# Kernel tuning notes

Hardware: AMD Instinct MI355X
Metric: run time of the kernel (lower is better)

## Reference

```python
import jax, jax.numpy as jnp
import numpy as np

VOCAB, T, IN, H, L = 32000, 4096, 512, 256, 2


def setup_inputs() -> dict:
    key = jax.random.key(0)
    ks = jax.random.split(key, 32)
    inp = {}
    inp["tokens"] = jax.random.randint(ks[0], (T,), 0, VOCAB)
    inp["emb"] = jax.random.normal(ks[1], (VOCAB, IN), dtype=jnp.float32) * 0.02
    i = 2
    for d in ("f", "b"):
        for l in range(L):
            in_l = IN if l == 0 else H
            inp[f"{d}_Wih{l}"] = jax.random.normal(ks[i], (4 * H, in_l), dtype=jnp.float32) * 0.05; i += 1
            inp[f"{d}_Whh{l}"] = jax.random.normal(ks[i], (4 * H, H), dtype=jnp.float32) * 0.05; i += 1
            inp[f"{d}_bih{l}"] = jnp.zeros((4 * H,), dtype=jnp.float32)
            inp[f"{d}_bhh{l}"] = jnp.zeros((4 * H,), dtype=jnp.float32)
    return inp


def _lstm_layer(x_seq, Wih, Whh, bih, bhh):
    # x_seq: [T, in]; torch.nn.LSTMCell gate order: i, f, g, o
    Hh = Whh.shape[1]
    b = bih + bhh
    def step(carry, x):
        h, c = carry
        g = x @ Wih.T + h @ Whh.T + b           # [4H]
        i_, f_, g_, o_ = jnp.split(g, 4)
        c = jax.nn.sigmoid(f_) * c + jax.nn.sigmoid(i_) * jnp.tanh(g_)
        h = jax.nn.sigmoid(o_) * jnp.tanh(c)
        return (h, c), h
    z = jnp.zeros((Hh,), x_seq.dtype)
    (h, c), hs = jax.lax.scan(step, (z, z), x_seq)
    return hs, h, c                              # [T,H], [H], [H]


def _run_dir(x_seq, params):
    finals = []
    h_seq = x_seq
    for (Wih, Whh, bih, bhh) in params:
        h_seq, h, c = _lstm_layer(h_seq, Wih, Whh, bih, bhh)
        finals.append((c, h))
    return h_seq, finals


def reference(tokens, emb,
              f_Wih0, f_Whh0, f_bih0, f_bhh0, f_Wih1, f_Whh1, f_bih1, f_bhh1,
              b_Wih0, b_Whh0, b_bih0, b_bhh0, b_Wih1, b_Whh1, b_bih1, b_bhh1):
    x = emb[tokens]                              # [T, IN] embedding lookup
    fparams = [(f_Wih0, f_Whh0, f_bih0, f_bhh0), (f_Wih1, f_Whh1, f_bih1, f_bhh1)]
    bparams = [(b_Wih0, b_Whh0, b_bih0, b_bhh0), (b_Wih1, b_Whh1, b_bih1, b_bhh1)]
    f_out, f_fin = _run_dir(x, fparams)          # forward over sequence
    b_out_rev, b_fin = _run_dir(x[::-1], bparams)  # backward over reversed sequence
    b_out = b_out_rev[::-1]
    outputs = jnp.concatenate([f_out, b_out], axis=-1)  # [T, 2H]
    cell_memories = jnp.stack([jnp.stack([f_fin[l][0], b_fin[l][0]]) for l in range(L)])  # [L,2,H]
    hidden_states = jnp.stack([jnp.stack([f_fin[l][1], b_fin[l][1]]) for l in range(L)])  # [L,2,H]
    return cell_memories, hidden_states, outputs
```

## Files before the change

kernel.cpp:

```cpp
#include <hip/hip_runtime.h>
#include <math.h>

#define T_SEQ 4096
#define NWG_LAUNCH 512

__device__ __forceinline__ float sigmoidf_(float x) {
  return 1.0f / (1.0f + expf(-x));
}

__device__ __forceinline__ unsigned long long pack_h(int tag, float h) {
  return ((unsigned long long)(unsigned)tag << 32) |
         (unsigned long long)__float_as_uint(h);
}

__device__ __forceinline__ unsigned long long ld_sc0(const unsigned long long* p) {
  unsigned long long v;
  asm volatile("global_load_dwordx2 %0, %1, off sc0\n\ts_waitcnt vmcnt(0)"
               : "=v"(v) : "v"(p) : "memory");
  return v;
}
__device__ __forceinline__ unsigned long long ld_mall(const unsigned long long* p) {
  unsigned long long v;
  asm volatile("global_load_dwordx2 %0, %1, off sc0 sc1\n\ts_waitcnt vmcnt(0)"
               : "=v"(v) : "v"(p) : "memory");
  return v;
}
__device__ __forceinline__ void st_pub(unsigned long long* p, unsigned long long v) {
  asm volatile("global_store_dwordx2 %0, %1, off sc0\n\t"
               "global_store_dwordx2 %0, %1, off sc0 sc1"
               :: "v"(p), "v"(v) : "memory");
}
__device__ __forceinline__ float poll_h(const unsigned long long* p, unsigned want) {
  int it = 0;
  for (;;) {
    unsigned long long v = ((it & 3) == 3) ? ld_mall(p) : ld_sc0(p);
    if ((unsigned)(v >> 32) == want) return __uint_as_float((unsigned)v);
    ++it;
  }
}

__global__ void gather_emb(const int* __restrict__ tokens,
                           const float4* __restrict__ emb4,
                           float4* __restrict__ X4) {
  int i = blockIdx.x * 256 + threadIdx.x;
  int t = i >> 7;
  int q = i & 127;
  X4[i] = emb4[(long)tokens[t] * 128 + q];
}

__global__ __launch_bounds__(256) void gemm_proj(
    const float* __restrict__ Xf, const float* __restrict__ Xb, int revb,
    const float* __restrict__ Wf, const float* __restrict__ Wb,
    const float* __restrict__ bihf, const float* __restrict__ bhhf,
    const float* __restrict__ bihb, const float* __restrict__ bhhb,
    float* __restrict__ Pf, float* __restrict__ Pb, int K)
{
  const int dirb = blockIdx.z;
  const float* X  = dirb ? Xb : Xf;
  const float* W  = dirb ? Wb : Wf;
  const float* bih = dirb ? bihb : bihf;
  const float* bhh = dirb ? bhhb : bhhf;
  float* Pp = dirb ? Pb : Pf;
  const int rev = dirb ? revb : 0;

  const int bn = blockIdx.x;
  const int bm = blockIdx.y;
  const int tid = threadIdx.x;
  const int tx = tid & 15, ty = tid >> 4;

  __shared__ float Xs[16][68];
  __shared__ float Ws[16][68];

  float acc[4][4] = {{0.f}};

  const int lrow = tid >> 2;
  const int lk4  = (tid & 3) * 4;
  const int xrow = bm * 64 + lrow;
  const int xsrc = rev ? (4095 - xrow) : xrow;
  const float* xptr = X + (long)xsrc * K + lk4;
  const float* wptr = W + (long)(bn * 64 + lrow) * K + lk4;

  for (int k0 = 0; k0 < K; k0 += 16) {
    float4 xv = *(const float4*)(xptr + k0);
    float4 wv = *(const float4*)(wptr + k0);
    __syncthreads();
    Xs[lk4 + 0][lrow] = xv.x; Xs[lk4 + 1][lrow] = xv.y;
    Xs[lk4 + 2][lrow] = xv.z; Xs[lk4 + 3][lrow] = xv.w;
    Ws[lk4 + 0][lrow] = wv.x; Ws[lk4 + 1][lrow] = wv.y;
    Ws[lk4 + 2][lrow] = wv.z; Ws[lk4 + 3][lrow] = wv.w;
    __syncthreads();
    #pragma unroll
    for (int kk = 0; kk < 16; ++kk) {
      float4 a = *(const float4*)(&Xs[kk][ty * 4]);
      float4 b = *(const float4*)(&Ws[kk][tx * 4]);
      acc[0][0] = fmaf(a.x, b.x, acc[0][0]); acc[0][1] = fmaf(a.x, b.y, acc[0][1]);
      acc[0][2] = fmaf(a.x, b.z, acc[0][2]); acc[0][3] = fmaf(a.x, b.w, acc[0][3]);
      acc[1][0] = fmaf(a.y, b.x, acc[1][0]); acc[1][1] = fmaf(a.y, b.y, acc[1][1]);
      acc[1][2] = fmaf(a.y, b.z, acc[1][2]); acc[1][3] = fmaf(a.y, b.w, acc[1][3]);
      acc[2][0] = fmaf(a.z, b.x, acc[2][0]); acc[2][1] = fmaf(a.z, b.y, acc[2][1]);
      acc[2][2] = fmaf(a.z, b.z, acc[2][2]); acc[2][3] = fmaf(a.z, b.w, acc[2][3]);
      acc[3][0] = fmaf(a.w, b.x, acc[3][0]); acc[3][1] = fmaf(a.w, b.y, acc[3][1]);
      acc[3][2] = fmaf(a.w, b.z, acc[3][2]); acc[3][3] = fmaf(a.w, b.w, acc[3][3]);
    }
  }

  const int c0 = bn * 64 + tx * 4;
  #pragma unroll
  for (int i = 0; i < 4; ++i) {
    const int r = bm * 64 + ty * 4 + i;
    float4 o4;
    o4.x = acc[i][0] + bih[c0 + 0] + bhh[c0 + 0];
    o4.y = acc[i][1] + bih[c0 + 1] + bhh[c0 + 1];
    o4.z = acc[i][2] + bih[c0 + 2] + bhh[c0 + 2];
    o4.w = acc[i][3] + bih[c0 + 3] + bhh[c0 + 3];
    *(float4*)(&Pp[(long)r * 1024 + c0]) = o4;
  }
}

__global__ __launch_bounds__(512, 2) void lstm_fused(
    const float* __restrict__ P0f, const float* __restrict__ P0b,
    const float* __restrict__ Whh0f, const float* __restrict__ Whh0b,
    const float* __restrict__ Wih1f, const float* __restrict__ Whh1f,
    const float* __restrict__ bih1f, const float* __restrict__ bhh1f,
    const float* __restrict__ Wih1b, const float* __restrict__ Whh1b,
    const float* __restrict__ bih1b, const float* __restrict__ bhh1b,
    float* __restrict__ out,
    unsigned long long* __restrict__ ring0,
    unsigned long long* __restrict__ h1x,
    int* __restrict__ flags)
{
  const int t = threadIdx.x;

  __shared__ int role_s;
  if (t == 0) {
    int xcd;
    asm volatile("s_getreg_b32 %0, hwreg(20, 0, 32)" : "=s"(xcd));
    xcd &= 7;
    int role = -1;
    const int lo = (xcd == 0) ? 0 : (xcd == 1 ? 12 : -1);
    if (lo >= 0) {
      for (int r = lo; r < lo + 12 && role < 0; ++r)
        if (atomicCAS(&flags[r], 0, 1) == 0) role = r;
    }
    const int n = atomicAdd(&flags[24], 1) + 1;
    if (role < 0 && n > NWG_LAUNCH - 32) {
      for (int r = 0; r < 24 && role < 0; ++r)
        if (atomicCAS(&flags[r], 0, 1) == 0) role = r;
    }
    role_s = role;
  }
  __syncthreads();
  const int role = role_s;
  if (role < 0) return;

  const int d   = role < 12 ? 0 : 1;
  const int sub = role < 12 ? role : role - 12;

  __shared__ float hx[512];
  __shared__ float lds_c[64];
  __shared__ float part[8 * 264];

  if (t < 64) lds_c[t] = 0.0f;

  unsigned long long* ring = ring0 + (long)d * T_SEQ * 256;

  if (sub < 4) {
    const int w = sub;
    const float* __restrict__ P = d ? P0b : P0f;
    const float* __restrict__ W = d ? Whh0b : Whh0f;

    const int kb = t >> 6;
    const int jg = t & 63;

    float wreg[128];
    #pragma unroll
    for (int jj = 0; jj < 4; ++jj) {
      const int m = jg * 4 + jj;
      const int j = (m >> 6) * 256 + w * 64 + (m & 63);
      const float4* wrow = (const float4*)(W + (long)j * 256 + kb * 32);
      #pragma unroll
      for (int kq = 0; kq < 8; ++kq) {
        float4 v = wrow[kq];
        wreg[jj * 32 + kq * 4 + 0] = v.x;
        wreg[jj * 32 + kq * 4 + 1] = v.y;
        wreg[jj * 32 + kq * 4 + 2] = v.z;
        wreg[jj * 32 + kq * 4 + 3] = v.w;
      }
    }

    const int cell = w * 64 + (t & 63);
    const long pbase = (long)(t & 63) + w * 64;

    for (int s = 0; s < T_SEQ; ++s) {
      float p0 = 0.f, p1 = 0.f, p2 = 0.f, p3 = 0.f;
      if (t < 64) {
        const float* prow = P + (long)s * 1024 + pbase;
        p0 = prow[0]; p1 = prow[256]; p2 = prow[512]; p3 = prow[768];
      }

      if (s == 0) {
        if (t < 256) hx[t] = 0.0f;
      } else if (t < 256) {
        hx[t] = poll_h(ring + (long)(s - 1) * 256 + t, (unsigned)s);
      }
      __syncthreads();

      float a0 = 0.f, a1 = 0.f, a2 = 0.f, a3 = 0.f;
      const float4* h4 = (const float4*)&hx[kb * 32];
      #pragma unroll
      for (int kq = 0; kq < 8; ++kq) {
        float4 hv = h4[kq];
        a0 = fmaf(wreg[0 * 32 + kq * 4 + 0], hv.x, a0);
        a0 = fmaf(wreg[0 * 32 + kq * 4 + 1], hv.y, a0);
        a0 = fmaf(wreg[0 * 32 + kq * 4 + 2], hv.z, a0);
        a0 = fmaf(wreg[0 * 32 + kq * 4 + 3], hv.w, a0);
        a1 = fmaf(wreg[1 * 32 + kq * 4 + 0], hv.x, a1);
        a1 = fmaf(wreg[1 * 32 + kq * 4 + 1], hv.y, a1);
        a1 = fmaf(wreg[1 * 32 + kq * 4 + 2], hv.z, a1);
        a1 = fmaf(wreg[1 * 32 + kq * 4 + 3], hv.w, a1);
        a2 = fmaf(wreg[2 * 32 + kq * 4 + 0], hv.x, a2);
        a2 = fmaf(wreg[2 * 32 + kq * 4 + 1], hv.y, a2);
        a2 = fmaf(wreg[2 * 32 + kq * 4 + 2], hv.z, a2);
        a2 = fmaf(wreg[2 * 32 + kq * 4 + 3], hv.w, a2);
        a3 = fmaf(wreg[3 * 32 + kq * 4 + 0], hv.x, a3);
        a3 = fmaf(wreg[3 * 32 + kq * 4 + 1], hv.y, a3);
        a3 = fmaf(wreg[3 * 32 + kq * 4 + 2], hv.z, a3);
        a3 = fmaf(wreg[3 * 32 + kq * 4 + 3], hv.w, a3);
      }
      float4 av; av.x = a0; av.y = a1; av.z = a2; av.w = a3;
      *(float4*)(&part[kb * 264 + jg * 4]) = av;
      __syncthreads();

      if (t < 64) {
        float s0 = p0, s1 = p1, s2 = p2, s3 = p3;
        #pragma unroll
        for (int q = 0; q < 8; ++q) {
          s0 += part[q * 264 + t];
          s1 += part[q * 264 + 64 + t];
          s2 += part[q * 264 + 128 + t];
          s3 += part[q * 264 + 192 + t];
        }
        float c = sigmoidf_(s1) * lds_c[t] + sigmoidf_(s0) * tanhf(s2);
        float h = sigmoidf_(s3) * tanhf(c);
        lds_c[t] = c;
        st_pub(ring + (long)s * 256 + cell, pack_h(s + 1, h));
        if (s == T_SEQ - 1) {
          out[d * 256 + cell] = c;
          out[1024 + d * 256 + cell] = h;
        }
      }
    }
  } else {
    const int w1 = sub - 4;
    const float* __restrict__ Wih = d ? Wih1b : Wih1f;
    const float* __restrict__ Whh = d ? Whh1b : Whh1f;
    const float* __restrict__ bih = d ? bih1b : bih1f;
    const float* __restrict__ bhh = d ? bhh1b : bhh1f;
    unsigned long long* slot = h1x + d * 512;
    float* hout = d ? (out + 2048 + (long)4095 * 512 + 256) : (out + 2048);
    const long hstr = d ? -512 : 512;

    const int kb = t >> 6;
    const int jg = t & 63;

    float wreg[2][64];
    #pragma unroll
    for (int rr = 0; rr < 2; ++rr) {
      const int m = jg * 2 + rr;
      const int j = (m >> 5) * 256 + w1 * 32 + (m & 31);
      const float* srcw = (kb < 4) ? (Wih + (long)j * 256 + kb * 64)
                                   : (Whh + (long)j * 256 + (kb - 4) * 64);
      const float4* s4 = (const float4*)srcw;
      #pragma unroll
      for (int q = 0; q < 16; ++q) {
        float4 v = s4[q];
        wreg[rr][q * 4 + 0] = v.x; wreg[rr][q * 4 + 1] = v.y;
        wreg[rr][q * 4 + 2] = v.z; wreg[rr][q * 4 + 3] = v.w;
      }
    }

    const int cell = w1 * 32 + (t & 31);
    float b0 = 0.f, b1 = 0.f, b2 = 0.f, b3 = 0.f;
    if (t < 32) {
      b0 = bih[cell] + bhh[cell];
      b1 = bih[256 + cell] + bhh[256 + cell];
      b2 = bih[512 + cell] + bhh[512 + cell];
      b3 = bih[768 + cell] + bhh[768 + cell];
    }

    for (int s = 0; s < T_SEQ; ++s) {
      if (t < 256) {
        hx[t] = poll_h(ring + (long)s * 256 + t, (unsigned)(s + 1));
      } else {
        hx[t] = poll_h(slot + ((s + 1) & 1) * 256 + (t - 256), (unsigned)s);
      }
      __syncthreads();

      float a0 = 0.f, a1 = 0.f;
      const float4* h4 = (const float4*)&hx[kb * 64];
      #pragma unroll
      for (int q = 0; q < 16; ++q) {
        float4 hv = h4[q];
        a0 = fmaf(wreg[0][q * 4 + 0], hv.x, a0);
        a0 = fmaf(wreg[0][q * 4 + 1], hv.y, a0);
        a0 = fmaf(wreg[0][q * 4 + 2], hv.z, a0);
        a0 = fmaf(wreg[0][q * 4 + 3], hv.w, a0);
        a1 = fmaf(wreg[1][q * 4 + 0], hv.x, a1);
        a1 = fmaf(wreg[1][q * 4 + 1], hv.y, a1);
        a1 = fmaf(wreg[1][q * 4 + 2], hv.z, a1);
        a1 = fmaf(wreg[1][q * 4 + 3], hv.w, a1);
      }
      float2 av2; av2.x = a0; av2.y = a1;
      *(float2*)(&part[kb * 264 + jg * 2]) = av2;
      __syncthreads();

      if (t < 32) {
        float s0 = b0, s1 = b1, s2 = b2, s3 = b3;
        #pragma unroll
        for (int q = 0; q < 8; ++q) {
          s0 += part[q * 264 + t];
          s1 += part[q * 264 + 32 + t];
          s2 += part[q * 264 + 64 + t];
          s3 += part[q * 264 + 96 + t];
        }
        float c = sigmoidf_(s1) * lds_c[t] + sigmoidf_(s0) * tanhf(s2);
        float h = sigmoidf_(s3) * tanhf(c);
        lds_c[t] = c;
        st_pub(&slot[(s & 1) * 256 + cell], pack_h(s + 1, h));
        hout[(long)s * hstr + cell] = h;
        if (s == T_SEQ - 1) {
          out[512 + d * 256 + cell] = c;
          out[1024 + 512 + d * 256 + cell] = h;
        }
      }
    }
  }
}

extern "C" void kernel_launch(void* const* d_in, const int* in_sizes, int n_in,
                              void* d_out, int out_size, void* d_ws, size_t ws_size,
                              hipStream_t stream) {
  const int*   tokens = (const int*)d_in[0];
  const float* emb    = (const float*)d_in[1];
  const float* fWih0 = (const float*)d_in[2];
  const float* fWhh0 = (const float*)d_in[3];
  const float* fbih0 = (const float*)d_in[4];
  const float* fbhh0 = (const float*)d_in[5];
  const float* fWih1 = (const float*)d_in[6];
  const float* fWhh1 = (const float*)d_in[7];
  const float* fbih1 = (const float*)d_in[8];
  const float* fbhh1 = (const float*)d_in[9];
  const float* bWih0 = (const float*)d_in[10];
  const float* bWhh0 = (const float*)d_in[11];
  const float* bbih0 = (const float*)d_in[12];
  const float* bbhh0 = (const float*)d_in[13];
  const float* bWih1 = (const float*)d_in[14];
  const float* bWhh1 = (const float*)d_in[15];
  const float* bbih1 = (const float*)d_in[16];
  const float* bbhh1 = (const float*)d_in[17];

  float* out = (float*)d_out;
  float* ws  = (float*)d_ws;

  float* X   = ws;
  float* P0f = ws + 4194304;
  float* P0b = ws + 8388608;
  unsigned long long* ring0 = (unsigned long long*)ws;
  unsigned long long* h1x   = (unsigned long long*)(ws + 12582912);
  int* flags = (int*)(ws + 12584960);

  gather_emb<<<2048, 256, 0, stream>>>(tokens, (const float4*)emb, (float4*)X);

  gemm_proj<<<dim3(16, 64, 2), 256, 0, stream>>>(
      X, X, 1, fWih0, bWih0, fbih0, fbhh0, bbih0, bbhh0, P0f, P0b, 512);

  hipMemsetAsync(ring0, 0, (size_t)2 * T_SEQ * 256 * sizeof(unsigned long long), stream);
  hipMemsetAsync(h1x, 0, 1024 * sizeof(unsigned long long) + 32 * sizeof(int), stream);

  lstm_fused<<<dim3(NWG_LAUNCH), 512, 0, stream>>>(
      P0f, P0b, fWhh0, bWhh0,
      fWih1, fWhh1, fbih1, fbhh1,
      bWih1, bWhh1, bbih1, bbhh1,
      out, ring0, h1x, flags);
}
```

Baseline: 7.026 ms.

## Double persistent LSTM workgroups per direction and parallelize gate activations

Splits each direction's recurrent work across 24 workgroups instead of 12: 8 for layer 0 with 32 cells each and 16 for layer 1 with 16 cells each. Each thread now holds fewer weight registers, and the gate nonlinearities are computed in parallel by 128 or 64 threads through a new LDS stage, with only the final c/h update serialized. The aim is to shorten the per-timestep critical path. In exchange it adds an extra barrier per step and more producer/consumer polling traffic across more workgroups. It also polls the MALL-level load less often.

```diff
diff --git a/kernel.cpp b/kernel.cpp
--- a/kernel.cpp
+++ b/kernel.cpp
@@ -3,6 +3,7 @@
 
 #define T_SEQ 4096
 #define NWG_LAUNCH 512
+#define NROLES 48
 
 __device__ __forceinline__ float sigmoidf_(float x) {
   return 1.0f / (1.0f + expf(-x));
@@ -33,7 +34,7 @@
 __device__ __forceinline__ float poll_h(const unsigned long long* p, unsigned want) {
   int it = 0;
   for (;;) {
-    unsigned long long v = ((it & 3) == 3) ? ld_mall(p) : ld_sc0(p);
+    unsigned long long v = ((it & 7) == 7) ? ld_mall(p) : ld_sc0(p);
     if ((unsigned)(v >> 32) == want) return __uint_as_float((unsigned)v);
     ++it;
   }
@@ -137,14 +138,14 @@
     asm volatile("s_getreg_b32 %0, hwreg(20, 0, 32)" : "=s"(xcd));
     xcd &= 7;
     int role = -1;
-    const int lo = (xcd == 0) ? 0 : (xcd == 1 ? 12 : -1);
+    const int lo = (xcd == 0) ? 0 : (xcd == 1 ? 24 : -1);
     if (lo >= 0) {
-      for (int r = lo; r < lo + 12 && role < 0; ++r)
+      for (int r = lo; r < lo + 24 && role < 0; ++r)
         if (atomicCAS(&flags[r], 0, 1) == 0) role = r;
     }
-    const int n = atomicAdd(&flags[24], 1) + 1;
-    if (role < 0 && n > NWG_LAUNCH - 32) {
-      for (int r = 0; r < 24 && role < 0; ++r)
+    const int n = atomicAdd(&flags[NROLES], 1) + 1;
+    if (role < 0 && n > NWG_LAUNCH - 64) {
+      for (int r = 0; r < NROLES && role < 0; ++r)
         if (atomicCAS(&flags[r], 0, 1) == 0) role = r;
     }
     role_s = role;
@@ -153,18 +154,19 @@
   const int role = role_s;
   if (role < 0) return;
 
-  const int d   = role < 12 ? 0 : 1;
-  const int sub = role < 12 ? role : role - 12;
+  const int d   = role < 24 ? 0 : 1;
+  const int sub = role % 24;
 
   __shared__ float hx[512];
+  __shared__ float part[8 * 132];
+  __shared__ float gact[128];
   __shared__ float lds_c[64];
-  __shared__ float part[8 * 264];
 
   if (t < 64) lds_c[t] = 0.0f;
 
   unsigned long long* ring = ring0 + (long)d * T_SEQ * 256;
 
-  if (sub < 4) {
+  if (sub < 8) {
     const int w = sub;
     const float* __restrict__ P = d ? P0b : P0f;
     const float* __restrict__ W = d ? Whh0b : Whh0f;
@@ -172,31 +174,26 @@
     const int kb = t >> 6;
     const int jg = t & 63;
 
-    float wreg[128];
+    float wreg[2][32];
     #pragma unroll
-    for (int jj = 0; jj < 4; ++jj) {
-      const int m = jg * 4 + jj;
-      const int j = (m >> 6) * 256 + w * 64 + (m & 63);
+    for (int rr = 0; rr < 2; ++rr) {
+      const int m = jg * 2 + rr;
+      const int j = (m >> 5) * 256 + w * 32 + (m & 31);
       const float4* wrow = (const float4*)(W + (long)j * 256 + kb * 32);
       #pragma unroll
       for (int kq = 0; kq < 8; ++kq) {
         float4 v = wrow[kq];
-        wreg[jj * 32 + kq * 4 + 0] = v.x;
-        wreg[jj * 32 + kq * 4 + 1] = v.y;
-        wreg[jj * 32 + kq * 4 + 2] = v.z;
-        wreg[jj * 32 + kq * 4 + 3] = v.w;
-      }
-    }
-
-    const int cell = w * 64 + (t & 63);
-    const long pbase = (long)(t & 63) + w * 64;
+        wreg[rr][kq * 4 + 0] = v.x; wreg[rr][kq * 4 + 1] = v.y;
+        wreg[rr][kq * 4 + 2] = v.z; wreg[rr][kq * 4 + 3] = v.w;
+      }
+    }
+
+    const int pj   = (t >> 5) * 256 + w * 32 + (t & 31);
+    const int cell = w * 32 + (t & 31);
 
     for (int s = 0; s < T_SEQ; ++s) {
-      float p0 = 0.f, p1 = 0.f, p2 = 0.f, p3 = 0.f;
-      if (t < 64) {
-        const float* prow = P + (long)s * 1024 + pbase;
-        p0 = prow[0]; p1 = prow[256]; p2 = prow[512]; p3 = prow[768];
-      }
+      float pval = 0.0f;
+      if (t < 128) pval = P[(long)s * 1024 + pj];
 
       if (s == 0) {
         if (t < 256) hx[t] = 0.0f;
@@ -205,43 +202,35 @@
       }
       __syncthreads();
 
-      float a0 = 0.f, a1 = 0.f, a2 = 0.f, a3 = 0.f;
+      float a0 = 0.f, a1 = 0.f;
       const float4* h4 = (const float4*)&hx[kb * 32];
       #pragma unroll
       for (int kq = 0; kq < 8; ++kq) {
         float4 hv = h4[kq];
-        a0 = fmaf(wreg[0 * 32 + kq * 4 + 0], hv.x, a0);
-        a0 = fmaf(wreg[0 * 32 + kq * 4 + 1], hv.y, a0);
-        a0 = fmaf(wreg[0 * 32 + kq * 4 + 2], hv.z, a0);
-        a0 = fmaf(wreg[0 * 32 + kq * 4 + 3], hv.w, a0);
-        a1 = fmaf(wreg[1 * 32 + kq * 4 + 0], hv.x, a1);
-        a1 = fmaf(wreg[1 * 32 + kq * 4 + 1], hv.y, a1);
-        a1 = fmaf(wreg[1 * 32 + kq * 4 + 2], hv.z, a1);
-        a1 = fmaf(wreg[1 * 32 + kq * 4 + 3], hv.w, a1);
-        a2 = fmaf(wreg[2 * 32 + kq * 4 + 0], hv.x, a2);
-        a2 = fmaf(wreg[2 * 32 + kq * 4 + 1], hv.y, a2);
-        a2 = fmaf(wreg[2 * 32 + kq * 4 + 2], hv.z, a2);
-        a2 = fmaf(wreg[2 * 32 + kq * 4 + 3], hv.w, a2);
-        a3 = fmaf(wreg[3 * 32 + kq * 4 + 0], hv.x, a3);
-        a3 = fmaf(wreg[3 * 32 + kq * 4 + 1], hv.y, a3);
-        a3 = fmaf(wreg[3 * 32 + kq * 4 + 2], hv.z, a3);
-        a3 = fmaf(wreg[3 * 32 + kq * 4 + 3], hv.w, a3);
-      }
-      float4 av; av.x = a0; av.y = a1; av.z = a2; av.w = a3;
-      *(float4*)(&part[kb * 264 + jg * 4]) = av;
-      __syncthreads();
-
-      if (t < 64) {
-        float s0 = p0, s1 = p1, s2 = p2, s3 = p3;
+        a0 = fmaf(wreg[0][kq * 4 + 0], hv.x, a0);
+        a0 = fmaf(wreg[0][kq * 4 + 1], hv.y, a0);
+        a0 = fmaf(wreg[0][kq * 4 + 2], hv.z, a0);
+        a0 = fmaf(wreg[0][kq * 4 + 3], hv.w, a0);
+        a1 = fmaf(wreg[1][kq * 4 + 0], hv.x, a1);
+        a1 = fmaf(wreg[1][kq * 4 + 1], hv.y, a1);
+        a1 = fmaf(wreg[1][kq * 4 + 2], hv.z, a1);
+        a1 = fmaf(wreg[1][kq * 4 + 3], hv.w, a1);
+      }
+      float2 av; av.x = a0; av.y = a1;
+      *(float2*)(&part[kb * 132 + jg * 2]) = av;
+      __syncthreads();
+
+      if (t < 128) {
+        float g = pval;
         #pragma unroll
-        for (int q = 0; q < 8; ++q) {
-          s0 += part[q * 264 + t];
-          s1 += part[q * 264 + 64 + t];
-          s2 += part[q * 264 + 128 + t];
-          s3 += part[q * 264 + 192 + t];
-        }
-        float c = sigmoidf_(s1) * lds_c[t] + sigmoidf_(s0) * tanhf(s2);
-        float h = sigmoidf_(s3) * tanhf(c);
+        for (int q = 0; q < 8; ++q) g += part[q * 132 + t];
+        gact[t] = ((t >> 5) == 2) ? tanhf(g) : sigmoidf_(g);
+      }
+      __syncthreads();
+
+      if (t < 32) {
+        float c = gact[32 + t] * lds_c[t] + gact[t] * gact[64 + t];
+        float h = gact[96 + t] * tanhf(c);
         lds_c[t] = c;
         st_pub(ring + (long)s * 256 + cell, pack_h(s + 1, h));
         if (s == T_SEQ - 1) {
@@ -251,7 +240,7 @@
       }
     }
   } else {
-    const int w1 = sub - 4;
+    const int w1 = sub - 8;
     const float* __restrict__ Wih = d ? Wih1b : Wih1f;
     const float* __restrict__ Whh = d ? Whh1b : Whh1f;
     const float* __restrict__ bih = d ? bih1b : bih1f;
@@ -261,32 +250,25 @@
     const long hstr = d ? -512 : 512;
 
     const int kb = t >> 6;
-    const int jg = t & 63;
-
-    float wreg[2][64];
-    #pragma unroll
-    for (int rr = 0; rr < 2; ++rr) {
-      const int m = jg * 2 + rr;
-      const int j = (m >> 5) * 256 + w1 * 32 + (m & 31);
+    const int m  = t & 63;
+
+    const int j = (m >> 4) * 256 + w1 * 16 + (m & 15);
+    float wreg[64];
+    {
       const float* srcw = (kb < 4) ? (Wih + (long)j * 256 + kb * 64)
                                    : (Whh + (long)j * 256 + (kb - 4) * 64);
       const float4* s4 = (const float4*)srcw;
       #pragma unroll
       for (int q = 0; q < 16; ++q) {
         float4 v = s4[q];
-        wreg[rr][q * 4 + 0] = v.x; wreg[rr][q * 4 + 1] = v.y;
-        wreg[rr][q * 4 + 2] = v.z; wreg[rr][q * 4 + 3] = v.w;
-      }
-    }
-
-    const int cell = w1 * 32 + (t & 31);
-    float b0 = 0.f, b1 = 0.f, b2 = 0.f, b3 = 0.f;
-    if (t < 32) {
-      b0 = bih[cell] + bhh[cell];
-      b1 = bih[256 + cell] + bhh[256 + cell];
-      b2 = bih[512 + cell] + bhh[512 + cell];
-      b3 = bih[768 + cell] + bhh[768 + cell];
-    }
+        wreg[q * 4 + 0] = v.x; wreg[q * 4 + 1] = v.y;
+        wreg[q * 4 + 2] = v.z; wreg[q * 4 + 3] = v.w;
+      }
+    }
+
+    const int cell = w1 * 16 + (t & 15);
+    float bsum = 0.0f;
+    if (t < 64) bsum = bih[j] + bhh[j];
 
     for (int s = 0; s < T_SEQ; ++s) {
       if (t < 256) {
@@ -299,32 +281,35 @@
       float a0 = 0.f, a1 = 0.f;
       const float4* h4 = (const float4*)&hx[kb * 64];
       #pragma unroll
-      for (int q = 0; q < 16; ++q) {
+      for (int q = 0; q < 8; ++q) {
         float4 hv = h4[q];
-        a0 = fmaf(wreg[0][q * 4 + 0], hv.x, a0);
-        a0 = fmaf(wreg[0][q * 4 + 1], hv.y, a0);
-        a0 = fmaf(wreg[0][q * 4 + 2], hv.z, a0);
-        a0 = fmaf(wreg[0][q * 4 + 3], hv.w, a0);
-        a1 = fmaf(wreg[1][q * 4 + 0], hv.x, a1);
-        a1 = fmaf(wreg[1][q * 4 + 1], hv.y, a1);
-        a1 = fmaf(wreg[1][q * 4 + 2], hv.z, a1);
-        a1 = fmaf(wreg[1][q * 4 + 3], hv.w, a1);
-      }
-      float2 av2; av2.x = a0; av2.y = a1;
-      *(float2*)(&part[kb * 264 + jg * 2]) = av2;
-      __syncthreads();
-
-      if (t < 32) {
-        float s0 = b0, s1 = b1, s2 = b2, s3 = b3;
+        a0 = fmaf(wreg[q * 4 + 0], hv.x, a0);
+        a0 = fmaf(wreg[q * 4 + 1], hv.y, a0);
+        a0 = fmaf(wreg[q * 4 + 2], hv.z, a0);
+        a0 = fmaf(wreg[q * 4 + 3], hv.w, a0);
+      }
+      #pragma unroll
+      for (int q = 8; q < 16; ++q) {
+        float4 hv = h4[q];
+        a1 = fmaf(wreg[q * 4 + 0], hv.x, a1);
+        a1 = fmaf(wreg[q * 4 + 1], hv.y, a1);
+        a1 = fmaf(wreg[q * 4 + 2], hv.z, a1);
+        a1 = fmaf(wreg[q * 4 + 3], hv.w, a1);
+      }
+      part[kb * 132 + m] = a0 + a1;
+      __syncthreads();
+
+      if (t < 64) {
+        float g = bsum;
         #pragma unroll
-        for (int q = 0; q < 8; ++q) {
-          s0 += part[q * 264 + t];
-          s1 += part[q * 264 + 32 + t];
-          s2 += part[q * 264 + 64 + t];
-          s3 += part[q * 264 + 96 + t];
-        }
-        float c = sigmoidf_(s1) * lds_c[t] + sigmoidf_(s0) * tanhf(s2);
-        float h = sigmoidf_(s3) * tanhf(c);
+        for (int q = 0; q < 8; ++q) g += part[q * 132 + t];
+        gact[t] = ((t >> 4) == 2) ? tanhf(g) : sigmoidf_(g);
+      }
+      __syncthreads();
+
+      if (t < 16) {
+        float c = gact[16 + t] * lds_c[t] + gact[t] * gact[32 + t];
+        float h = gact[48 + t] * tanhf(c);
         lds_c[t] = c;
         st_pub(&slot[(s & 1) * 256 + cell], pack_h(s + 1, h));
         hout[(long)s * hstr + cell] = h;
@@ -375,7 +360,7 @@
       X, X, 1, fWih0, bWih0, fbih0, fbhh0, bbih0, bbhh0, P0f, P0b, 512);
 
   hipMemsetAsync(ring0, 0, (size_t)2 * T_SEQ * 256 * sizeof(unsigned long long), stream);
-  hipMemsetAsync(h1x, 0, 1024 * sizeof(unsigned long long) + 32 * sizeof(int), stream);
+  hipMemsetAsync(h1x, 0, 1024 * sizeof(unsigned long long) + 64 * sizeof(int), stream);
 
   lstm_fused<<<dim3(NWG_LAUNCH), 512, 0, stream>>>(
       P0f, P0b, fWhh0, bWhh0,
```

Result: slower. 9.386 ms (+33.6%).
